# Kernel tuning notes

Measured on AMD Instinct MI355X. Metric: run time of the kernel, lower is better.

## Reference

```python
import jax, jax.numpy as jnp
import numpy as np

B, S, C, H = 8, 1024, 768, 8
D = C // H  # head dim = 96
MLP = 4 * C


def setup_inputs() -> dict:
    key = jax.random.key(0)
    ks = jax.random.split(key, 12)
    sc = 0.02
    return {
        "x": jax.random.normal(ks[0], (B, S, C), jnp.float32),
        "ln1_w": jnp.ones((S, C), jnp.float32),
        "ln1_b": jnp.zeros((S, C), jnp.float32),
        "ln2_w": jnp.ones((S, C), jnp.float32),
        "ln2_b": jnp.zeros((S, C), jnp.float32),
        "qkv_w": jax.random.normal(ks[1], (C, 3 * C), jnp.float32) * sc,
        "proj_w": jax.random.normal(ks[2], (C, C), jnp.float32) * sc,
        "mlp_w1": jax.random.normal(ks[3], (C, MLP), jnp.float32) * sc,
        "mlp_b1": jnp.zeros((MLP,), jnp.float32),
        "mlp_w2": jax.random.normal(ks[4], (MLP, C), jnp.float32) * sc,
        "mlp_b2": jnp.zeros((C,), jnp.float32),
    }


def _layernorm2d(x, w, b, eps=1e-5):
    # normalizes over BOTH (seq, channel) dims, per nn.LayerNorm([length, channel])
    mu = jnp.mean(x, axis=(-2, -1), keepdims=True)
    var = jnp.mean(jnp.square(x - mu), axis=(-2, -1), keepdims=True)
    return (x - mu) * jax.lax.rsqrt(var + eps) * w + b


def _attention(x, qkv_w, proj_w):
    b, s, _ = x.shape
    qkv = (x @ qkv_w).reshape(b, s, 3, H, D)
    q, k, v = qkv[:, :, 0], qkv[:, :, 1], qkv[:, :, 2]  # [b, s, h, d]
    # NOTE: original module applies NO 1/sqrt(d) scaling
    scores = jnp.einsum("bshd,bthd->bhst", q, k)
    attn = jax.nn.softmax(scores, axis=-1)
    out = jnp.einsum("bhst,bthd->bshd", attn, v).reshape(b, s, C)
    return out @ proj_w


def reference(x, ln1_w, ln1_b, ln2_w, ln2_b, qkv_w, proj_w, mlp_w1, mlp_b1, mlp_w2, mlp_b2):
    # dropout is identity in eval mode
    h = x + _attention(_layernorm2d(x, ln1_w, ln1_b), qkv_w, proj_w)
    y = _layernorm2d(h, ln2_w, ln2_b)
    y = jax.nn.gelu(y @ mlp_w1 + mlp_b1, approximate=False)
    return h + (y @ mlp_w2 + mlp_b2)
```

## Files before the change

### kernel.cpp

```cpp
#include <hip/hip_runtime.h>
#include <hip/hip_bf16.h>

#define S_LEN 1024
#define NB 8
#define NC 768
#define NH 8
#define HD 96
#define NMLP 3072
#define SC (S_LEN*NC)
#define BS (NB*S_LEN)

typedef __attribute__((ext_vector_type(8))) unsigned short u16x8;
typedef __attribute__((ext_vector_type(4))) unsigned short u16x4;
typedef __attribute__((ext_vector_type(8))) __bf16 bf16x8;
typedef __attribute__((ext_vector_type(4))) float f32x4;

__device__ __forceinline__ unsigned short f2b(float f) {
  union { __hip_bfloat16 h; unsigned short u; } cvt;
  cvt.h = __float2bfloat16(f);
  return cvt.u;
}

__device__ __forceinline__ void gload16(const unsigned short* g, unsigned short* l) {
  __builtin_amdgcn_global_load_lds(
      (const __attribute__((address_space(1))) unsigned int*)g,
      (__attribute__((address_space(3))) unsigned int*)l, 16, 0, 0);
}

template<int EPI>
__global__ __launch_bounds__(256, 2)
void gemm_bt(const unsigned short* __restrict__ A, int lda,
             const unsigned short* __restrict__ Bt, int ldb,
             void* __restrict__ Cv, int ldc,
             int K,
             const float* __restrict__ bias,
             const float* __restrict__ residual, int ldr)
{
  __shared__ unsigned short As[128*32];
  __shared__ unsigned short Bs[128*32];
  const int tid = threadIdx.x;
  const int lane = tid & 63;
  const int wid = tid >> 6;
  const int wm = wid & 1, wn = wid >> 1;
  const int r15 = lane & 15, g = lane >> 4;
  const int tm = blockIdx.x * 128;
  const int tn = blockIdx.y * 128;

  const unsigned short* Ab = A  + (size_t)(tm + wid*32 + (lane>>2))*lda + (lane&3)*8;
  const unsigned short* Bb = Bt + (size_t)(tn + wid*32 + (lane>>2))*ldb + (lane&3)*8;

  f32x4 acc[4][4];
  #pragma unroll
  for (int m = 0; m < 4; ++m)
    #pragma unroll
    for (int n = 0; n < 4; ++n)
      acc[m][n] = (f32x4){0.f, 0.f, 0.f, 0.f};

  for (int k0 = 0; k0 < K; k0 += 32) {
    gload16(Ab + k0,                    As + (wid*2 + 0)*512);
    gload16(Ab + (size_t)16*lda + k0,   As + (wid*2 + 1)*512);
    gload16(Bb + k0,                    Bs + (wid*2 + 0)*512);
    gload16(Bb + (size_t)16*ldb + k0,   Bs + (wid*2 + 1)*512);
    __syncthreads();
    bf16x8 af[4], bfr[4];
    #pragma unroll
    for (int m = 0; m < 4; ++m)
      af[m] = *(const bf16x8*)(As + (wm*64 + m*16 + r15)*32 + g*8);
    #pragma unroll
    for (int n = 0; n < 4; ++n)
      bfr[n] = *(const bf16x8*)(Bs + (wn*64 + n*16 + r15)*32 + g*8);
    #pragma unroll
    for (int m = 0; m < 4; ++m)
      #pragma unroll
      for (int n = 0; n < 4; ++n)
        acc[m][n] = __builtin_amdgcn_mfma_f32_16x16x32_bf16(af[m], bfr[n], acc[m][n], 0, 0, 0);
    __syncthreads();
  }

  unsigned short* Cu = (unsigned short*)Cv;
  float* Cf = (float*)Cv;
  #pragma unroll
  for (int m = 0; m < 4; ++m) {
    #pragma unroll
    for (int n = 0; n < 4; ++n) {
      const int col = tn + wn*64 + n*16 + r15;
      #pragma unroll
      for (int r = 0; r < 4; ++r) {
        const int row = tm + wm*64 + m*16 + g*4 + r;
        float v = acc[m][n][r];
        if (EPI == 2 || EPI == 4) v += bias[col];
        if (EPI == 3 || EPI == 4) v += residual[(size_t)row*ldr + col];
        if (EPI == 2) v = 0.5f*v*(1.0f + erff(v*0.70710678118654752f));
        if (EPI == 0 || EPI == 2) Cu[(size_t)row*ldc + col] = f2b(v);
        else                      Cf[(size_t)row*ldc + col] = v;
      }
    }
  }
}

__global__ __launch_bounds__(256, 2)
void flash_attn(const unsigned short* __restrict__ qkv,
                const unsigned short* __restrict__ vt,
                unsigned short* __restrict__ outb)
{
  __shared__ unsigned short Ks[128*96];
  __shared__ unsigned short Vs[96*128];
  __shared__ unsigned short Ps[128*128];
  const int tid = threadIdx.x, lane = tid & 63, wq = tid >> 6;
  const int r15 = lane & 15, g = lane >> 4;
  const int bh = blockIdx.y, b = bh >> 3, h = bh & 7;
  const int q0 = blockIdx.x * 128;
  const int swz = (r15 & 7) << 4;
  char* PsB = (char*)Ps;
  char* VsB = (char*)Vs;

  bf16x8 qf[2][3];
  {
    const unsigned short* qb = qkv + ((size_t)b*S_LEN + q0 + wq*32 + r15)*2304 + h*HD + g*8;
    #pragma unroll
    for (int n = 0; n < 2; ++n)
      #pragma unroll
      for (int kc = 0; kc < 3; ++kc)
        qf[n][kc] = *(const bf16x8*)(qb + (size_t)n*16*2304 + kc*32);
  }

  int krow[6], kcol[6], vrow[6], vcol[6];
  #pragma unroll
  for (int i = 0; i < 6; ++i) {
    const int c = (wq*6 + i)*64 + lane;
    krow[i] = c / 12;
    kcol[i] = (c % 12) * 8;
    const int L = c * 16;
    const int row = L >> 8, cb = L & 255;
    vrow[i] = row;
    vcol[i] = (cb ^ ((row & 7) << 4)) >> 1;
  }
  const unsigned short* kbase = qkv + (size_t)b*S_LEN*2304 + NC + h*HD;
  const unsigned short* vbase = vt + (size_t)bh*HD*S_LEN;

  f32x4 oacc[6][2];
  #pragma unroll
  for (int m = 0; m < 6; ++m) {
    oacc[m][0] = (f32x4){0.f,0.f,0.f,0.f};
    oacc[m][1] = (f32x4){0.f,0.f,0.f,0.f};
  }
  float mrun[2] = {-INFINITY, -INFINITY};
  float lrun[2] = {0.f, 0.f};

  for (int kt = 0; kt < 8; ++kt) {
    const unsigned short* ksrc = kbase + (size_t)kt*128*2304;
    const unsigned short* vsrc = vbase + kt*128;
    #pragma unroll
    for (int i = 0; i < 6; ++i) {
      gload16(ksrc + (size_t)krow[i]*2304 + kcol[i], Ks + (wq*6 + i)*512);
      gload16(vsrc + vrow[i]*1024 + vcol[i],         Vs + (wq*6 + i)*512);
    }
    __syncthreads();

    f32x4 sacc[8][2];
    #pragma unroll
    for (int m = 0; m < 8; ++m) {
      sacc[m][0] = (f32x4){0.f,0.f,0.f,0.f};
      sacc[m][1] = (f32x4){0.f,0.f,0.f,0.f};
    }
    #pragma unroll
    for (int kc = 0; kc < 3; ++kc)
      #pragma unroll
      for (int m = 0; m < 8; ++m) {
        bf16x8 kf = *(const bf16x8*)(Ks + (m*16 + r15)*96 + kc*32 + g*8);
        sacc[m][0] = __builtin_amdgcn_mfma_f32_16x16x32_bf16(kf, qf[0][kc], sacc[m][0], 0,0,0);
        sacc[m][1] = __builtin_amdgcn_mfma_f32_16x16x32_bf16(kf, qf[1][kc], sacc[m][1], 0,0,0);
      }

    #pragma unroll
    for (int n = 0; n < 2; ++n) {
      float pm = -INFINITY;
      #pragma unroll
      for (int m = 0; m < 8; ++m)
        #pragma unroll
        for (int r = 0; r < 4; ++r) pm = fmaxf(pm, sacc[m][n][r]);
      pm = fmaxf(pm, __shfl_xor(pm, 16));
      pm = fmaxf(pm, __shfl_xor(pm, 32));
      const float newm = fmaxf(mrun[n], pm);
      const float scale = __expf(mrun[n] - newm);
      mrun[n] = newm;
      const int qloc = wq*32 + n*16 + r15;
      float s = 0.f;
      #pragma unroll
      for (int m = 0; m < 8; ++m) {
        float e0 = __expf(sacc[m][n][0] - newm);
        float e1 = __expf(sacc[m][n][1] - newm);
        float e2 = __expf(sacc[m][n][2] - newm);
        float e3 = __expf(sacc[m][n][3] - newm);
        s += (e0 + e1) + (e2 + e3);
        u16x4 pk = { f2b(e0), f2b(e1), f2b(e2), f2b(e3) };
        *(u16x4*)(PsB + ((qloc*256 + m*32 + g*8) ^ swz)) = pk;
      }
      s += __shfl_xor(s, 16);
      s += __shfl_xor(s, 32);
      lrun[n] = lrun[n]*scale + s;
      #pragma unroll
      for (int m = 0; m < 6; ++m) oacc[m][n] *= scale;
    }

    #pragma unroll
    for (int kc = 0; kc < 4; ++kc) {
      bf16x8 pf0 = *(const bf16x8*)(PsB + (((wq*32      + r15)*256 + kc*64 + g*16) ^ swz));
      bf16x8 pf1 = *(const bf16x8*)(PsB + (((wq*32 + 16 + r15)*256 + kc*64 + g*16) ^ swz));
      #pragma unroll
      for (int m = 0; m < 6; ++m) {
        bf16x8 vf = *(const bf16x8*)(VsB + (((m*16 + r15)*256 + kc*64 + g*16) ^ swz));
        oacc[m][0] = __builtin_amdgcn_mfma_f32_16x16x32_bf16(vf, pf0, oacc[m][0], 0,0,0);
        oacc[m][1] = __builtin_amdgcn_mfma_f32_16x16x32_bf16(vf, pf1, oacc[m][1], 0,0,0);
      }
    }
    __syncthreads();
  }

  #pragma unroll
  for (int n = 0; n < 2; ++n) {
    const float inv = 1.0f / lrun[n];
    unsigned short* orow = outb + ((size_t)b*S_LEN + q0 + wq*32 + n*16 + r15)*NC + h*HD;
    #pragma unroll
    for (int m = 0; m < 6; ++m) {
      u16x4 pk = { f2b(oacc[m][n][0]*inv), f2b(oacc[m][n][1]*inv),
                   f2b(oacc[m][n][2]*inv), f2b(oacc[m][n][3]*inv) };
      *(u16x4*)(orow + m*16 + g*4) = pk;
    }
  }
}

__global__ void transpose_cast(const float* __restrict__ W, unsigned short* __restrict__ Wt,
                               int K, int N)
{
  __shared__ float tile[32][33];
  const int tx = threadIdx.x & 31, ty = threadIdx.x >> 5;
  const int n0 = blockIdx.x * 32, k0 = blockIdx.y * 32;
  #pragma unroll
  for (int i = 0; i < 32; i += 8)
    tile[ty + i][tx] = W[(size_t)(k0 + ty + i)*N + n0 + tx];
  __syncthreads();
  #pragma unroll
  for (int i = 0; i < 32; i += 8)
    Wt[(size_t)(n0 + ty + i)*K + k0 + tx] = f2b(tile[tx][ty + i]);
}

__global__ void transpose_v(const unsigned short* __restrict__ qkv, unsigned short* __restrict__ vt)
{
  __shared__ unsigned short tile[32][33];
  const int bh = blockIdx.z, b = bh >> 3, h = bh & 7;
  const unsigned short* v = qkv + (size_t)b*S_LEN*3*NC + 2*NC + h*HD;
  unsigned short* o = vt + (size_t)bh*HD*S_LEN;
  const int s0 = blockIdx.x * 32, d0 = blockIdx.y * 32;
  const int tx = threadIdx.x & 31, ty = threadIdx.x >> 5;
  #pragma unroll
  for (int i = 0; i < 32; i += 8)
    tile[ty + i][tx] = v[(size_t)(s0 + ty + i)*(3*NC) + d0 + tx];
  __syncthreads();
  #pragma unroll
  for (int i = 0; i < 32; i += 8)
    o[(size_t)(d0 + ty + i)*S_LEN + s0 + tx] = tile[tx][ty + i];
}

__global__ void ln_part(const float* __restrict__ X, float* __restrict__ part)
{
  const int b = blockIdx.x / 96, blk = blockIdx.x % 96;
  const float4* xb = (const float4*)(X + (size_t)b*SC);
  float s = 0.f, s2 = 0.f;
  #pragma unroll
  for (int i = 0; i < 8; ++i) {
    float4 v = xb[blk*2048 + i*256 + threadIdx.x];
    s  += v.x + v.y + v.z + v.w;
    s2 += v.x*v.x + v.y*v.y + v.z*v.z + v.w*v.w;
  }
  #pragma unroll
  for (int o = 32; o; o >>= 1) { s += __shfl_down(s, o); s2 += __shfl_down(s2, o); }
  __shared__ float r1[4], r2[4];
  const int w = threadIdx.x >> 6;
  if ((threadIdx.x & 63) == 0) { r1[w] = s; r2[w] = s2; }
  __syncthreads();
  if (threadIdx.x == 0) {
    part[(b*96 + blk)*2]     = r1[0] + r1[1] + r1[2] + r1[3];
    part[(b*96 + blk)*2 + 1] = r2[0] + r2[1] + r2[2] + r2[3];
  }
}

__global__ void ln_fin(const float* __restrict__ part, float* __restrict__ stats)
{
  const int b = blockIdx.x;
  float s = 0.f, s2 = 0.f;
  for (int i = threadIdx.x; i < 96; i += 64) {
    s  += part[(b*96 + i)*2];
    s2 += part[(b*96 + i)*2 + 1];
  }
  #pragma unroll
  for (int o = 32; o; o >>= 1) { s += __shfl_down(s, o); s2 += __shfl_down(s2, o); }
  if (threadIdx.x == 0) {
    const float inv = 1.0f / (float)SC;
    const float mu = s * inv;
    const float var = s2 * inv - mu*mu;
    stats[b*2] = mu;
    stats[b*2 + 1] = rsqrtf(var + 1e-5f);
  }
}

__global__ void ln_apply(const float* __restrict__ X, const float* __restrict__ W,
                         const float* __restrict__ Bv, const float* __restrict__ stats,
                         unsigned short* __restrict__ out)
{
  const size_t i = ((size_t)blockIdx.x*256 + threadIdx.x) * 8;
  const int b = (int)(i / SC);
  const size_t r = i % SC;
  const float mu = stats[b*2], rs = stats[b*2 + 1];
  float4 x0 = *(const float4*)(X + i),  x1 = *(const float4*)(X + i + 4);
  float4 w0 = *(const float4*)(W + r),  w1 = *(const float4*)(W + r + 4);
  float4 b0 = *(const float4*)(Bv + r), b1 = *(const float4*)(Bv + r + 4);
  u16x8 o;
  o[0] = f2b((x0.x - mu)*rs*w0.x + b0.x);
  o[1] = f2b((x0.y - mu)*rs*w0.y + b0.y);
  o[2] = f2b((x0.z - mu)*rs*w0.z + b0.z);
  o[3] = f2b((x0.w - mu)*rs*w0.w + b0.w);
  o[4] = f2b((x1.x - mu)*rs*w1.x + b1.x);
  o[5] = f2b((x1.y - mu)*rs*w1.y + b1.y);
  o[6] = f2b((x1.z - mu)*rs*w1.z + b1.z);
  o[7] = f2b((x1.w - mu)*rs*w1.w + b1.w);
  *(u16x8*)(out + i) = o;
}

extern "C" void kernel_launch(void* const* d_in, const int* in_sizes, int n_in,
                              void* d_out, int out_size, void* d_ws, size_t ws_size,
                              hipStream_t stream) {
  const float* x      = (const float*)d_in[0];
  const float* ln1_w  = (const float*)d_in[1];
  const float* ln1_b  = (const float*)d_in[2];
  const float* ln2_w  = (const float*)d_in[3];
  const float* ln2_b  = (const float*)d_in[4];
  const float* qkv_w  = (const float*)d_in[5];
  const float* proj_w = (const float*)d_in[6];
  const float* mlp_w1 = (const float*)d_in[7];
  const float* mlp_b1 = (const float*)d_in[8];
  const float* mlp_w2 = (const float*)d_in[9];
  const float* mlp_b2 = (const float*)d_in[10];
  float* out = (float*)d_out;

  char* ws = (char*)d_ws;
  size_t off = 0;
  auto alloc = [&](size_t b) { size_t o = off; off += (b + 255) & ~(size_t)255; return o; };
  unsigned short* wqkvT  = (unsigned short*)(ws + alloc((size_t)3*NC*NC*2));
  unsigned short* wprojT = (unsigned short*)(ws + alloc((size_t)NC*NC*2));
  unsigned short* w1T    = (unsigned short*)(ws + alloc((size_t)NMLP*NC*2));
  unsigned short* w2T    = (unsigned short*)(ws + alloc((size_t)NC*NMLP*2));
  unsigned short* lnbf   = (unsigned short*)(ws + alloc((size_t)BS*NC*2));
  const size_t qkvOff    = alloc((size_t)BS*3*NC*2);
  unsigned short* qkvbf  = (unsigned short*)(ws + qkvOff);
  unsigned short* vt     = (unsigned short*)(ws + alloc((size_t)NB*NH*HD*S_LEN*2));
  unsigned short* ybf    = (unsigned short*)(ws + qkvOff);
  float* hbuf            = (float*)(ws + alloc((size_t)BS*NC*4));
  float* part            = (float*)(ws + alloc((size_t)NB*96*2*4));
  float* stats           = (float*)(ws + alloc((size_t)NB*2*4));
  (void)ws_size; (void)in_sizes; (void)n_in; (void)out_size;

  const dim3 blk(256);

  transpose_cast<<<dim3(3*NC/32, NC/32),   blk, 0, stream>>>(qkv_w,  wqkvT,  NC, 3*NC);
  transpose_cast<<<dim3(NC/32, NC/32),     blk, 0, stream>>>(proj_w, wprojT, NC, NC);
  transpose_cast<<<dim3(NMLP/32, NC/32),   blk, 0, stream>>>(mlp_w1, w1T,    NC, NMLP);
  transpose_cast<<<dim3(NC/32, NMLP/32),   blk, 0, stream>>>(mlp_w2, w2T,    NMLP, NC);

  ln_part<<<dim3(NB*96), blk, 0, stream>>>(x, part);
  ln_fin<<<dim3(NB), dim3(64), 0, stream>>>(part, stats);
  ln_apply<<<dim3(BS*NC/2048), blk, 0, stream>>>(x, ln1_w, ln1_b, stats, lnbf);

  gemm_bt<0><<<dim3(BS/128, 3*NC/128), blk, 0, stream>>>(
      lnbf, NC, wqkvT, NC, qkvbf, 3*NC, NC, nullptr, nullptr, 0);

  transpose_v<<<dim3(S_LEN/32, HD/32, NB*NH), blk, 0, stream>>>(qkvbf, vt);

  flash_attn<<<dim3(S_LEN/128, NB*NH), blk, 0, stream>>>(qkvbf, vt, lnbf);

  gemm_bt<3><<<dim3(BS/128, NC/128), blk, 0, stream>>>(
      lnbf, NC, wprojT, NC, hbuf, NC, NC, nullptr, x, NC);

  ln_part<<<dim3(NB*96), blk, 0, stream>>>(hbuf, part);
  ln_fin<<<dim3(NB), dim3(64), 0, stream>>>(part, stats);
  ln_apply<<<dim3(BS*NC/2048), blk, 0, stream>>>(hbuf, ln2_w, ln2_b, stats, lnbf);

  gemm_bt<2><<<dim3(BS/128, NMLP/128), blk, 0, stream>>>(
      lnbf, NC, w1T, NC, ybf, NMLP, NC, mlp_b1, nullptr, 0);

  gemm_bt<4><<<dim3(BS/128, NC/128), blk, 0, stream>>>(
      ybf, NMLP, w2T, NMLP, out, NC, NMLP, mlp_b2, hbuf, NC);
}
```

Measured before the change: 298.9 us.

## Rewrite GEMM as 128x256 double-buffered kernel, fuse LN2 stats, tanh GELU

Replaces the 128x128 single-buffered GEMM with a 512-thread 128x256-tile kernel. It uses K=64 steps, double-buffered swizzled LDS loads, explicit vmcnt waits and setprio around the MFMA blocks. The projection GEMM epilogue now accumulates sum and sum-of-squares for the second layernorm through atomics, which removes the separate ln_part/ln_fin passes. Exact erf GELU is replaced by a tanh approximation, and setprio is also added in flash attention. The one-pass variance (E[x^2]-mu^2) and the tanh GELU change numerics, and the atomics make the reduction order nondeterministic.

Result: faster. 287.3 us (-3.9%).

```diff
diff --git a/kernel.cpp b/kernel.cpp
--- a/kernel.cpp
+++ b/kernel.cpp
@@ -27,73 +27,122 @@
       (__attribute__((address_space(3))) unsigned int*)l, 16, 0, 0);
 }
 
+__device__ __forceinline__ float gelu_f(float v) {
+  float u = v * (0.7978845608f + 0.0356774081f * v * v);
+  float au = fabsf(u);
+  float e = __expf(-2.0f * au);
+  float th = (1.0f - e) / (1.0f + e);
+  th = copysignf(th, u);
+  return 0.5f * v * (1.0f + th);
+}
+
 template<int EPI>
-__global__ __launch_bounds__(256, 2)
-void gemm_bt(const unsigned short* __restrict__ A, int lda,
-             const unsigned short* __restrict__ Bt, int ldb,
-             void* __restrict__ Cv, int ldc,
-             int K,
-             const float* __restrict__ bias,
-             const float* __restrict__ residual, int ldr)
-{
-  __shared__ unsigned short As[128*32];
-  __shared__ unsigned short Bs[128*32];
-  const int tid = threadIdx.x;
-  const int lane = tid & 63;
-  const int wid = tid >> 6;
-  const int wm = wid & 1, wn = wid >> 1;
+__global__ __launch_bounds__(512, 1)
+void gemmks(const unsigned short* __restrict__ A, int lda,
+            const unsigned short* __restrict__ Bt, int ldb,
+            void* __restrict__ Cv, int ldc, int K,
+            const float* __restrict__ bias,
+            const float* __restrict__ residual, int ldr,
+            float* __restrict__ lnred)
+{
+  __shared__ unsigned short As[4*4096];
+  __shared__ unsigned short Bs[4*8192];
+  const int tid = threadIdx.x, lane = tid & 63, wid = tid >> 6;
   const int r15 = lane & 15, g = lane >> 4;
-  const int tm = blockIdx.x * 128;
-  const int tn = blockIdx.y * 128;
-
-  const unsigned short* Ab = A  + (size_t)(tm + wid*32 + (lane>>2))*lda + (lane&3)*8;
-  const unsigned short* Bb = Bt + (size_t)(tn + wid*32 + (lane>>2))*ldb + (lane&3)*8;
-
-  f32x4 acc[4][4];
-  #pragma unroll
-  for (int m = 0; m < 4; ++m)
-    #pragma unroll
-    for (int n = 0; n < 4; ++n)
-      acc[m][n] = (f32x4){0.f, 0.f, 0.f, 0.f};
-
-  for (int k0 = 0; k0 < K; k0 += 32) {
-    gload16(Ab + k0,                    As + (wid*2 + 0)*512);
-    gload16(Ab + (size_t)16*lda + k0,   As + (wid*2 + 1)*512);
-    gload16(Bb + k0,                    Bs + (wid*2 + 0)*512);
-    gload16(Bb + (size_t)16*ldb + k0,   Bs + (wid*2 + 1)*512);
-    __syncthreads();
-    bf16x8 af[4], bfr[4];
-    #pragma unroll
-    for (int m = 0; m < 4; ++m)
-      af[m] = *(const bf16x8*)(As + (wm*64 + m*16 + r15)*32 + g*8);
-    #pragma unroll
-    for (int n = 0; n < 4; ++n)
-      bfr[n] = *(const bf16x8*)(Bs + (wn*64 + n*16 + r15)*32 + g*8);
-    #pragma unroll
-    for (int m = 0; m < 4; ++m)
-      #pragma unroll
-      for (int n = 0; n < 4; ++n)
-        acc[m][n] = __builtin_amdgcn_mfma_f32_16x16x32_bf16(af[m], bfr[n], acc[m][n], 0, 0, 0);
-    __syncthreads();
-  }
+  const int tm = blockIdx.x * 128, tn = blockIdx.y * 256;
+  const int NT = K >> 6;
+
+  const int sa = lane >> 3, sc = lane & 7, slc = sc ^ sa;
+  const int skc = (slc & 3) << 3;
+  const int arow = wid*16 + sa*2 + ((slc >> 2) & 1);
+  const unsigned short* Ag  = A  + (size_t)(tm + arow)*lda + skc;
+  const unsigned short* Bg0 = Bt + (size_t)(tn + arow)*ldb + skc;
+  const unsigned short* Bg1 = Bt + (size_t)(tn + 128 + arow)*ldb + skc;
+
+  const int prl = r15 >> 1;
+  const int rdo = prl*128 + (((((r15 & 1) << 2) | g) ^ prl) << 4);
+  char* AsB = (char*)As; char* BsB = (char*)Bs;
+
+#define STG(h,kk,b) { \
+    gload16(Ag  + (kk) + (h)*32, As + ((b)*2+(h))*4096 + wid*512); \
+    gload16(Bg0 + (kk) + (h)*32, Bs + ((b)*2+(h))*8192 + wid*512); \
+    gload16(Bg1 + (kk) + (h)*32, Bs + ((b)*2+(h))*8192 + 4096 + wid*512); }
+#define MFMA(a8,b8,c) __builtin_amdgcn_mfma_f32_16x16x32_bf16(a8,b8,c,0,0,0)
+
+  f32x4 acc[8][2];
+  #pragma unroll
+  for (int m = 0; m < 8; ++m) {
+    acc[m][0] = (f32x4){0.f,0.f,0.f,0.f};
+    acc[m][1] = (f32x4){0.f,0.f,0.f,0.f};
+  }
+
+  STG(0,0,0); STG(1,0,0);
+
+  for (int t = 0; t < NT; ++t) {
+    const int rd = t & 1, wr = rd ^ 1;
+    const int kk = (t + 1) << 6;
+    const bool pre = (t + 1) < NT;
+    #pragma unroll
+    for (int h = 0; h < 2; ++h) {
+      if (pre || h == 0) asm volatile("s_waitcnt vmcnt(3)" ::: "memory");
+      else               asm volatile("s_waitcnt vmcnt(0)" ::: "memory");
+      __builtin_amdgcn_s_barrier();
+      const int ab = (rd*2 + h)*8192;
+      const int bb = (rd*2 + h)*16384;
+      bf16x8 a[8], b[2];
+      #pragma unroll
+      for (int m = 0; m < 8; ++m) a[m] = *(const bf16x8*)(AsB + ab + m*1024 + rdo);
+      b[0] = *(const bf16x8*)(BsB + bb + wid*2048 + rdo);
+      b[1] = *(const bf16x8*)(BsB + bb + wid*2048 + 1024 + rdo);
+      if (pre) STG(h, kk, wr);
+      asm volatile("s_waitcnt lgkmcnt(0)" ::: "memory");
+      __builtin_amdgcn_s_setprio(1);
+      #pragma unroll
+      for (int m = 0; m < 8; ++m) {
+        acc[m][0] = MFMA(a[m], b[0], acc[m][0]);
+        acc[m][1] = MFMA(a[m], b[1], acc[m][1]);
+      }
+      __builtin_amdgcn_s_setprio(0);
+    }
+  }
+#undef STG
+#undef MFMA
 
   unsigned short* Cu = (unsigned short*)Cv;
   float* Cf = (float*)Cv;
-  #pragma unroll
-  for (int m = 0; m < 4; ++m) {
-    #pragma unroll
-    for (int n = 0; n < 4; ++n) {
-      const int col = tn + wn*64 + n*16 + r15;
+  float s1 = 0.f, s2 = 0.f;
+  #pragma unroll
+  for (int m = 0; m < 8; ++m) {
+    #pragma unroll
+    for (int n = 0; n < 2; ++n) {
+      const int col = tn + wid*32 + n*16 + r15;
       #pragma unroll
       for (int r = 0; r < 4; ++r) {
-        const int row = tm + wm*64 + m*16 + g*4 + r;
+        const int row = tm + m*16 + g*4 + r;
         float v = acc[m][n][r];
         if (EPI == 2 || EPI == 4) v += bias[col];
         if (EPI == 3 || EPI == 4) v += residual[(size_t)row*ldr + col];
-        if (EPI == 2) v = 0.5f*v*(1.0f + erff(v*0.70710678118654752f));
+        if (EPI == 2) v = gelu_f(v);
+        if (EPI == 3) { s1 += v; s2 += v*v; }
         if (EPI == 0 || EPI == 2) Cu[(size_t)row*ldc + col] = f2b(v);
         else                      Cf[(size_t)row*ldc + col] = v;
       }
+    }
+  }
+  if (EPI == 3) {
+    #pragma unroll
+    for (int o = 32; o; o >>= 1) { s1 += __shfl_xor(s1, o); s2 += __shfl_xor(s2, o); }
+    __syncthreads();
+    float* red = (float*)As;
+    if (lane == 0) { red[wid*2] = s1; red[wid*2+1] = s2; }
+    __syncthreads();
+    if (tid == 0) {
+      float a1 = 0.f, a2 = 0.f;
+      #pragma unroll
+      for (int w = 0; w < 8; ++w) { a1 += red[w*2]; a2 += red[w*2+1]; }
+      const int bidx = tm >> 10;
+      atomicAdd(&lnred[bidx*2],     a1);
+      atomicAdd(&lnred[bidx*2 + 1], a2);
     }
   }
 }
@@ -163,6 +212,7 @@
       sacc[m][0] = (f32x4){0.f,0.f,0.f,0.f};
       sacc[m][1] = (f32x4){0.f,0.f,0.f,0.f};
     }
+    __builtin_amdgcn_s_setprio(1);
     #pragma unroll
     for (int kc = 0; kc < 3; ++kc)
       #pragma unroll
@@ -171,6 +221,7 @@
         sacc[m][0] = __builtin_amdgcn_mfma_f32_16x16x32_bf16(kf, qf[0][kc], sacc[m][0], 0,0,0);
         sacc[m][1] = __builtin_amdgcn_mfma_f32_16x16x32_bf16(kf, qf[1][kc], sacc[m][1], 0,0,0);
       }
+    __builtin_amdgcn_s_setprio(0);
 
     #pragma unroll
     for (int n = 0; n < 2; ++n) {
@@ -207,12 +258,14 @@
     for (int kc = 0; kc < 4; ++kc) {
       bf16x8 pf0 = *(const bf16x8*)(PsB + (((wq*32      + r15)*256 + kc*64 + g*16) ^ swz));
       bf16x8 pf1 = *(const bf16x8*)(PsB + (((wq*32 + 16 + r15)*256 + kc*64 + g*16) ^ swz));
+      __builtin_amdgcn_s_setprio(1);
       #pragma unroll
       for (int m = 0; m < 6; ++m) {
         bf16x8 vf = *(const bf16x8*)(VsB + (((m*16 + r15)*256 + kc*64 + g*16) ^ swz));
         oacc[m][0] = __builtin_amdgcn_mfma_f32_16x16x32_bf16(vf, pf0, oacc[m][0], 0,0,0);
         oacc[m][1] = __builtin_amdgcn_mfma_f32_16x16x32_bf16(vf, pf1, oacc[m][1], 0,0,0);
       }
+      __builtin_amdgcn_s_setprio(0);
     }
     __syncthreads();
   }
@@ -327,6 +380,32 @@
   *(u16x8*)(out + i) = o;
 }
 
+__global__ void ln_apply_f(const float* __restrict__ X, const float* __restrict__ W,
+                           const float* __restrict__ Bv, const float* __restrict__ red,
+                           unsigned short* __restrict__ out)
+{
+  const size_t i = ((size_t)blockIdx.x*256 + threadIdx.x) * 8;
+  const int b = (int)(i / SC);
+  const size_t r = i % SC;
+  const float inv = 1.0f / (float)SC;
+  const float mu = red[b*2] * inv;
+  const float var = red[b*2 + 1] * inv - mu*mu;
+  const float rs = rsqrtf(var + 1e-5f);
+  float4 x0 = *(const float4*)(X + i),  x1 = *(const float4*)(X + i + 4);
+  float4 w0 = *(const float4*)(W + r),  w1 = *(const float4*)(W + r + 4);
+  float4 b0 = *(const float4*)(Bv + r), b1 = *(const float4*)(Bv + r + 4);
+  u16x8 o;
+  o[0] = f2b((x0.x - mu)*rs*w0.x + b0.x);
+  o[1] = f2b((x0.y - mu)*rs*w0.y + b0.y);
+  o[2] = f2b((x0.z - mu)*rs*w0.z + b0.z);
+  o[3] = f2b((x0.w - mu)*rs*w0.w + b0.w);
+  o[4] = f2b((x1.x - mu)*rs*w1.x + b1.x);
+  o[5] = f2b((x1.y - mu)*rs*w1.y + b1.y);
+  o[6] = f2b((x1.z - mu)*rs*w1.z + b1.z);
+  o[7] = f2b((x1.w - mu)*rs*w1.w + b1.w);
+  *(u16x8*)(out + i) = o;
+}
+
 extern "C" void kernel_launch(void* const* d_in, const int* in_sizes, int n_in,
                               void* d_out, int out_size, void* d_ws, size_t ws_size,
                               hipStream_t stream) {
@@ -358,9 +437,13 @@
   float* hbuf            = (float*)(ws + alloc((size_t)BS*NC*4));
   float* part            = (float*)(ws + alloc((size_t)NB*96*2*4));
   float* stats           = (float*)(ws + alloc((size_t)NB*2*4));
+  float* lnred           = (float*)(ws + alloc((size_t)NB*2*4));
   (void)ws_size; (void)in_sizes; (void)n_in; (void)out_size;
 
   const dim3 blk(256);
+  const dim3 blk512(512);
+
+  hipMemsetAsync(lnred, 0, NB*2*sizeof(float), stream);
 
   transpose_cast<<<dim3(3*NC/32, NC/32),   blk, 0, stream>>>(qkv_w,  wqkvT,  NC, 3*NC);
   transpose_cast<<<dim3(NC/32, NC/32),     blk, 0, stream>>>(proj_w, wprojT, NC, NC);
@@ -371,23 +454,21 @@
   ln_fin<<<dim3(NB), dim3(64), 0, stream>>>(part, stats);
   ln_apply<<<dim3(BS*NC/2048), blk, 0, stream>>>(x, ln1_w, ln1_b, stats, lnbf);
 
-  gemm_bt<0><<<dim3(BS/128, 3*NC/128), blk, 0, stream>>>(
-      lnbf, NC, wqkvT, NC, qkvbf, 3*NC, NC, nullptr, nullptr, 0);
+  gemmks<0><<<dim3(BS/128, 3*NC/256), blk512, 0, stream>>>(
+      lnbf, NC, wqkvT, NC, qkvbf, 3*NC, NC, nullptr, nullptr, 0, nullptr);
 
   transpose_v<<<dim3(S_LEN/32, HD/32, NB*NH), blk, 0, stream>>>(qkvbf, vt);
 
   flash_attn<<<dim3(S_LEN/128, NB*NH), blk, 0, stream>>>(qkvbf, vt, lnbf);
 
-  gemm_bt<3><<<dim3(BS/128, NC/128), blk, 0, stream>>>(
-      lnbf, NC, wprojT, NC, hbuf, NC, NC, nullptr, x, NC);
-
-  ln_part<<<dim3(NB*96), blk, 0, stream>>>(hbuf, part);
-  ln_fin<<<dim3(NB), dim3(64), 0, stream>>>(part, stats);
-  ln_apply<<<dim3(BS*NC/2048), blk, 0, stream>>>(hbuf, ln2_w, ln2_b, stats, lnbf);
-
-  gemm_bt<2><<<dim3(BS/128, NMLP/128), blk, 0, stream>>>(
-      lnbf, NC, w1T, NC, ybf, NMLP, NC, mlp_b1, nullptr, 0);
-
-  gemm_bt<4><<<dim3(BS/128, NC/128), blk, 0, stream>>>(
-      ybf, NMLP, w2T, NMLP, out, NC, NMLP, mlp_b2, hbuf, NC);
-}
+  gemmks<3><<<dim3(BS/128, NC/256), blk512, 0, stream>>>(
+      lnbf, NC, wprojT, NC, hbuf, NC, NC, nullptr, x, NC, lnred);
+
+  ln_apply_f<<<dim3(BS*NC/2048), blk, 0, stream>>>(hbuf, ln2_w, ln2_b, lnred, lnbf);
+
+  gemmks<2><<<dim3(BS/128, NMLP/256), blk512, 0, stream>>>(
+      lnbf, NC, w1T, NC, ybf, NMLP, NC, mlp_b1, nullptr, 0, nullptr);
+
+  gemmks<4><<<dim3(BS/128, NC/256), blk512, 0, stream>>>(
+      ybf, NMLP, w2T, NMLP, out, NC, NMLP, mlp_b2, hbuf, NC, nullptr);
+}
```
